# Optimization experiments

Hardware: AMD Instinct MI355X
Metric: run time of the kernel (lower is better)

The kernel has to match this reference:

```python
import jax, jax.numpy as jnp
import numpy as np

B, T, D, H = 8, 4096, 1024, 1024


def setup_inputs() -> dict:
    key = jax.random.key(0)
    ks = jax.random.split(key, 8)
    s = 1.0 / np.sqrt(D)
    x = jax.random.normal(ks[0], (B, T, D), dtype=jnp.float32)
    Wq = jax.random.uniform(ks[1], (H, D), jnp.float32, -s, s)
    bq = jax.random.uniform(ks[2], (H,), jnp.float32, -s, s)
    Wk = jax.random.uniform(ks[3], (H, D), jnp.float32, -s, s)
    bk = jax.random.uniform(ks[4], (H,), jnp.float32, -s, s)
    Wv = jax.random.uniform(ks[5], (H, D), jnp.float32, -s, s)
    bv = jax.random.uniform(ks[6], (H,), jnp.float32, -s, s)
    wbias = jax.random.uniform(ks[7], (H,), jnp.float32, 0.0, 1.0)  # torch.rand
    return {"x": x, "Wq": Wq, "bq": bq, "Wk": Wk, "bk": bk, "Wv": Wv, "bv": bv, "wbias": wbias}


def reference(x, Wq, bq, Wk, bk, Wv, bv, wbias):
    # Q, K, V: [B, T, H]
    Q = jnp.einsum('btd,hd->bth', x, Wq) + bq
    K = jnp.einsum('btd,hd->bth', x, Wk) + bk
    V = jnp.einsum('btd,hd->bth', x, Wv) + bv
    Q_sig = jax.nn.sigmoid(Q)
    numer = jnp.exp(K + wbias)            # [B, T, H]
    denom = numer.sum(axis=0)             # [T, H] (faithful: sum over batch axis)
    weighted = (numer * V).sum(axis=0) / denom  # [T, H]
    Yt = Q_sig * weighted                 # broadcast -> [B, T, H]
    return Yt  # to_out is Identity since dim == hidden_dim
```

## Files before the change

### kernel.cpp

```cpp
#include <hip/hip_runtime.h>
#include <hip/hip_bf16.h>

#define B_ 8
#define T_ 4096
#define D_ 1024
#define H_ 1024

typedef __attribute__((ext_vector_type(8))) short short8;
typedef __attribute__((ext_vector_type(4))) float floatx4;

#define GLOAD16(gptr, lptr) \
  __builtin_amdgcn_global_load_lds((const __attribute__((address_space(1))) void*)(gptr), \
                                   (__attribute__((address_space(3))) void*)(lptr), 16, 0, 0)

__device__ __forceinline__ ushort f2b(float f) {
  unsigned x = __builtin_bit_cast(unsigned, f);
  unsigned r = (x + 0x7fffu + ((x >> 16) & 1u)) >> 16;
  return (ushort)r;
}

__global__ void cvt_kernel(const float* __restrict__ in, ushort* __restrict__ out, int n) {
  int idx = blockIdx.x * blockDim.x + threadIdx.x;
  int stride = gridDim.x * blockDim.x;
  for (long i = (long)idx * 8; i < n; i += (long)stride * 8) {
    const float4 f0 = *(const float4*)(in + i);
    const float4 f1 = *(const float4*)(in + i + 4);
    union { ushort u[8]; uint4 v; } r;
    r.u[0] = f2b(f0.x); r.u[1] = f2b(f0.y); r.u[2] = f2b(f0.z); r.u[3] = f2b(f0.w);
    r.u[4] = f2b(f1.x); r.u[5] = f2b(f1.y); r.u[6] = f2b(f1.z); r.u[7] = f2b(f1.w);
    *(uint4*)(out + i) = r.v;
  }
}

__global__ void cvt3_kernel(const float* __restrict__ w0, const float* __restrict__ w1,
                            const float* __restrict__ w2, ushort* __restrict__ out, int n) {
  const float* in = (blockIdx.y == 0) ? w0 : (blockIdx.y == 1) ? w1 : w2;
  ushort* o = out + (size_t)blockIdx.y * n;
  int idx = blockIdx.x * blockDim.x + threadIdx.x;
  int stride = gridDim.x * blockDim.x;
  for (long i = (long)idx * 8; i < n; i += (long)stride * 8) {
    const float4 f0 = *(const float4*)(in + i);
    const float4 f1 = *(const float4*)(in + i + 4);
    union { ushort u[8]; uint4 v; } r;
    r.u[0] = f2b(f0.x); r.u[1] = f2b(f0.y); r.u[2] = f2b(f0.z); r.u[3] = f2b(f0.w);
    r.u[4] = f2b(f1.x); r.u[5] = f2b(f1.y); r.u[6] = f2b(f1.z); r.u[7] = f2b(f1.w);
    *(uint4*)(o + i) = r.v;
  }
}

__global__ __launch_bounds__(512, 2) void kv_kernel(
    const ushort* __restrict__ xb, const ushort* __restrict__ Wkb,
    const ushort* __restrict__ Wvb, const float* __restrict__ bk,
    const float* __restrict__ bv, const float* __restrict__ wbias,
    float* __restrict__ weighted) {
  extern __shared__ ushort lds[];
  ushort* const AsB = lds;
  ushort* const KsB = lds + 49152;
  ushort* const VsB = lds + 61440;

  const int tid = threadIdx.x;
  const int lane = tid & 63;
  const int w = tid >> 6;
  const int wrow = w >> 1;
  const int wcol = w & 1;

  const int bid = blockIdx.x;
  const int lid = (bid & 7) * 32 + (bid >> 3);
  const int t0 = (lid >> 4) * 256;
  const int h0 = (lid & 15) * 64;

  const int srow = tid >> 3;
  const int swz = (tid & 7) ^ ((tid >> 3) & 7);

  const int arow = wrow * 64 + (lane & 15);
  const int bcol = wcol * 32 + (lane & 15);
  const int cs0 = (lane >> 4) ^ (lane & 7);
  const int cs1 = ((lane >> 4) + 4) ^ (lane & 7);

  float wbc[2], bkc[2], bvc[2];
#pragma unroll
  for (int n = 0; n < 2; ++n) {
    int h = h0 + wcol * 32 + n * 16 + (lane & 15);
    wbc[n] = wbias[h];
    bkc[n] = bk[h];
    bvc[n] = bv[h];
  }

  const ushort* xsb = xb + (size_t)(t0 + srow) * D_ + swz * 8;
  const ushort* ksb = Wkb + (size_t)(h0 + srow) * D_ + swz * 8;
  const ushort* vsb = Wvb + (size_t)(h0 + srow) * D_ + swz * 8;

  auto stage = [&](int p, int nb) {
    const int b = p >> 4;
    const int kt = (p & 15) << 6;
    const ushort* xs = xsb + (size_t)b * (T_ * D_) + kt;
    ushort* Ab = AsB + nb * 16384;
#pragma unroll
    for (int it = 0; it < 4; ++it)
      GLOAD16(xs + (size_t)(it * 64) * D_, Ab + (it * 512 + tid) * 8);
    GLOAD16(ksb + kt, KsB + nb * 4096 + tid * 8);
    GLOAD16(vsb + kt, VsB + nb * 4096 + tid * 8);
  };

  floatx4 accK[4][2] = {};
  floatx4 accV[4][2] = {};
  floatx4 sumN[4][2] = {};
  floatx4 sumWV[4][2] = {};

  stage(0, 0);
  stage(1, 1);
  asm volatile("s_waitcnt vmcnt(6)" ::: "memory");
  __builtin_amdgcn_s_barrier();

  int cur = 0, stg = 2;
  for (int p = 0; p < 128; ++p) {
    if (p < 126) stage(p + 2, stg);

    const ushort* Ac = AsB + cur * 16384;
    const ushort* Kc = KsB + cur * 4096;
    const ushort* Vc = VsB + cur * 4096;
#pragma unroll
    for (int s = 0; s < 2; ++s) {
      const int cs = s ? cs1 : cs0;
      short8 a[4], kb2[2], vb2[2];
#pragma unroll
      for (int m = 0; m < 4; ++m)
        a[m] = *(const short8*)&Ac[(arow + m * 16) * 64 + cs * 8];
#pragma unroll
      for (int n = 0; n < 2; ++n) {
        kb2[n] = *(const short8*)&Kc[(bcol + n * 16) * 64 + cs * 8];
        vb2[n] = *(const short8*)&Vc[(bcol + n * 16) * 64 + cs * 8];
      }
      __builtin_amdgcn_s_setprio(1);
#pragma unroll
      for (int m = 0; m < 4; ++m)
#pragma unroll
        for (int n = 0; n < 2; ++n) {
          accK[m][n] = __builtin_amdgcn_mfma_f32_16x16x32_bf16(a[m], kb2[n], accK[m][n], 0, 0, 0);
          accV[m][n] = __builtin_amdgcn_mfma_f32_16x16x32_bf16(a[m], vb2[n], accV[m][n], 0, 0, 0);
        }
      __builtin_amdgcn_s_setprio(0);
    }

    if ((p & 15) == 15) {
#pragma unroll
      for (int m = 0; m < 4; ++m)
#pragma unroll
        for (int n = 0; n < 2; ++n) {
#pragma unroll
          for (int r = 0; r < 4; ++r) {
            float nmr = __expf(accK[m][n][r] + bkc[n] + wbc[n]);
            sumN[m][n][r] += nmr;
            sumWV[m][n][r] += nmr * (accV[m][n][r] + bvc[n]);
          }
          accK[m][n] = floatx4{0.f, 0.f, 0.f, 0.f};
          accV[m][n] = floatx4{0.f, 0.f, 0.f, 0.f};
        }
    }

    if (p < 126) { asm volatile("s_waitcnt vmcnt(6)" ::: "memory"); }
    else         { asm volatile("s_waitcnt vmcnt(0)" ::: "memory"); }
    __builtin_amdgcn_s_barrier();
    cur = (cur == 2) ? 0 : cur + 1;
    stg = (stg == 2) ? 0 : stg + 1;
  }

#pragma unroll
  for (int m = 0; m < 4; ++m)
#pragma unroll
    for (int n = 0; n < 2; ++n)
#pragma unroll
      for (int r = 0; r < 4; ++r) {
        int t = t0 + wrow * 64 + m * 16 + (lane >> 4) * 4 + r;
        int h = h0 + wcol * 32 + n * 16 + (lane & 15);
        weighted[(size_t)t * H_ + h] = sumWV[m][n][r] / sumN[m][n][r];
      }
}

__global__ __launch_bounds__(512, 2) void q_kernel(
    const ushort* __restrict__ Am, const ushort* __restrict__ Bm,
    const float* __restrict__ bq, const float* __restrict__ weighted,
    float* __restrict__ out) {
  extern __shared__ ushort lds[];

  const int tid = threadIdx.x;
  const int lane = tid & 63;
  const int w = tid >> 6;
  const int wr = w >> 2;
  const int wc = w & 3;

  const int bid = blockIdx.x;
  const int lid = (bid & 7) * 64 + (bid >> 3);
  const int R0 = (lid >> 2) * 256;
  const int C0 = (lid & 3) * 256;

  const int r0 = tid >> 2;
  const int lc = (tid & 3) ^ ((tid >> 3) & 3);
  const ushort* asrc = Am + (size_t)(R0 + r0) * D_ + lc * 8;
  const ushort* bsrc = Bm + (size_t)(C0 + r0) * D_ + lc * 8;

  auto stage = [&](int t) {
    const int nb = t & 3;
    const int kt = t * 32;
    GLOAD16(asrc + kt, lds + nb * 8192 + tid * 8);
    GLOAD16(asrc + kt + (size_t)128 * D_, lds + nb * 8192 + (512 + tid) * 8);
    GLOAD16(bsrc + kt, lds + 32768 + nb * 8192 + tid * 8);
    GLOAD16(bsrc + kt + (size_t)128 * D_, lds + 32768 + nb * 8192 + (512 + tid) * 8);
  };

  const int baseA = wr * 128 + (lane & 15);
  const int baseB = wc * 64 + (lane & 15);
  const int aOff = baseA * 32 + ((lane >> 4) ^ ((baseA >> 1) & 3)) * 8;
  const int bOff = baseB * 32 + ((lane >> 4) ^ ((baseB >> 1) & 3)) * 8;

  floatx4 acc[8][4] = {};

  stage(0); stage(1);
  asm volatile("s_waitcnt vmcnt(4)" ::: "memory");
  __builtin_amdgcn_s_barrier();

  const int NT = D_ / 32;
  for (int t = 0; t < NT; ++t) {
    if (t < NT - 2) stage(t + 2);
    const ushort* Ab = lds + (t & 3) * 8192;
    const ushort* Bb = lds + 32768 + (t & 3) * 8192;

    short8 b[4], a[8];
#pragma unroll
    for (int n = 0; n < 4; ++n) b[n] = *(const short8*)(Bb + bOff + n * 512);
#pragma unroll
    for (int m = 0; m < 8; ++m) a[m] = *(const short8*)(Ab + aOff + m * 512);
#pragma unroll
    for (int m = 0; m < 8; ++m)
#pragma unroll
      for (int n = 0; n < 4; ++n)
        acc[m][n] = __builtin_amdgcn_mfma_f32_16x16x32_bf16(a[m], b[n], acc[m][n], 0, 0, 0);

    if (t < NT - 2) { asm volatile("s_waitcnt vmcnt(4)" ::: "memory"); }
    else            { asm volatile("s_waitcnt vmcnt(0)" ::: "memory"); }
    __builtin_amdgcn_s_barrier();
  }

  const int lrb = wr * 64 + (lane >> 4) * 4;
  const int lcol = wc * 64 + (lane & 15);
#pragma unroll
  for (int mh = 0; mh < 2; ++mh) {
    if (mh) __builtin_amdgcn_s_barrier();
    float* lf = (float*)lds;
#pragma unroll
    for (int mi = 0; mi < 4; ++mi)
#pragma unroll
      for (int n = 0; n < 4; ++n)
#pragma unroll
        for (int r = 0; r < 4; ++r)
          lf[(lrb + mi * 16 + r) * 256 + lcol + n * 16] = acc[mh * 4 + mi][n][r];
    __builtin_amdgcn_s_barrier();
#pragma unroll
    for (int j = 0; j < 16; ++j) {
      int cidx = j * 512 + tid;
      int lr = cidx >> 6;
      int cc = cidx & 63;
      int grow = R0 + (lr >> 6) * 128 + mh * 64 + (lr & 63);
      float4 v = *(float4*)(lf + lr * 256 + cc * 4);
      float4 bq4 = *(const float4*)(bq + C0 + cc * 4);
      float4 wv = *(const float4*)(weighted + (size_t)(grow & (T_ - 1)) * H_ + C0 + cc * 4);
      float4 o;
      o.x = wv.x / (1.f + __expf(-(v.x + bq4.x)));
      o.y = wv.y / (1.f + __expf(-(v.y + bq4.y)));
      o.z = wv.z / (1.f + __expf(-(v.z + bq4.z)));
      o.w = wv.w / (1.f + __expf(-(v.w + bq4.w)));
      *(float4*)(out + (size_t)grow * H_ + C0 + cc * 4) = o;
    }
  }
}

extern "C" void kernel_launch(void* const* d_in, const int* in_sizes, int n_in,
                              void* d_out, int out_size, void* d_ws, size_t ws_size,
                              hipStream_t stream) {
  (void)in_sizes; (void)n_in; (void)out_size; (void)ws_size;
  const float* x = (const float*)d_in[0];
  const float* Wq = (const float*)d_in[1];
  const float* bq = (const float*)d_in[2];
  const float* Wk = (const float*)d_in[3];
  const float* bk = (const float*)d_in[4];
  const float* Wv = (const float*)d_in[5];
  const float* bv = (const float*)d_in[6];
  const float* wbias = (const float*)d_in[7];
  float* out = (float*)d_out;

  char* ws = (char*)d_ws;
  const size_t XN = (size_t)B_ * T_ * D_;
  const size_t WN = (size_t)H_ * D_;
  ushort* xb  = (ushort*)ws;
  ushort* Wqb = (ushort*)(ws + XN * 2);
  ushort* Wkb = Wqb + WN;
  ushort* Wvb = Wkb + WN;
  float* weighted = (float*)(ws + XN * 2 + 3 * WN * 2);

  (void)hipFuncSetAttribute((const void*)kv_kernel,
                            hipFuncAttributeMaxDynamicSharedMemorySize, 147456);
  (void)hipFuncSetAttribute((const void*)q_kernel,
                            hipFuncAttributeMaxDynamicSharedMemorySize, 131072);

  cvt_kernel<<<2048, 256, 0, stream>>>(x, xb, (int)XN);
  cvt3_kernel<<<dim3(512, 3), 256, 0, stream>>>(Wq, Wk, Wv, Wqb, (int)WN);

  kv_kernel<<<256, 512, 147456, stream>>>(xb, Wkb, Wvb, bk, bv, wbias, weighted);
  q_kernel<<<512, 512, 131072, stream>>>(xb, Wqb, bq, weighted, out);
}
```

Baseline: 276.9 us.

## Restage kv_kernel K-tiles to 32 wide covering two batches per stage

```diff
diff --git a/kernel.cpp b/kernel.cpp
--- a/kernel.cpp
+++ b/kernel.cpp
@@ -55,8 +55,7 @@
     float* __restrict__ weighted) {
   extern __shared__ ushort lds[];
   ushort* const AsB = lds;
-  ushort* const KsB = lds + 49152;
-  ushort* const VsB = lds + 61440;
+  ushort* const BsB = lds + 49152;
 
   const int tid = threadIdx.x;
   const int lane = tid & 63;
@@ -69,13 +68,30 @@
   const int t0 = (lid >> 4) * 256;
   const int h0 = (lid & 15) * 64;
 
-  const int srow = tid >> 3;
-  const int swz = (tid & 7) ^ ((tid >> 3) & 7);
-
-  const int arow = wrow * 64 + (lane & 15);
-  const int bcol = wcol * 32 + (lane & 15);
-  const int cs0 = (lane >> 4) ^ (lane & 7);
-  const int cs1 = ((lane >> 4) + 4) ^ (lane & 7);
+  const int rA = tid >> 2;
+  const int lcA = (tid & 3) ^ ((tid >> 3) & 3);
+  const int ci = tid & 255;
+  const int rB = ci >> 2;
+  const int lcB = (ci & 3) ^ ((ci >> 3) & 3);
+
+  const ushort* xsb = xb + (size_t)(t0 + rA) * D_ + lcA * 8;
+  const ushort* wsrc = ((tid < 256) ? Wkb : Wvb) + (size_t)(h0 + rB) * D_ + lcB * 8;
+
+  auto stage = [&](int p, int buf) {
+    const int b0 = (p >> 5) * 2;
+    const int kt = (p & 31) << 5;
+    const ushort* x0 = xsb + (size_t)b0 * (T_ * D_) + kt;
+    ushort* Ab = AsB + buf * 16384;
+    GLOAD16(x0, Ab + tid * 8);
+    GLOAD16(x0 + (size_t)128 * D_, Ab + (512 + tid) * 8);
+    GLOAD16(x0 + (size_t)(T_ * D_), Ab + (1024 + tid) * 8);
+    GLOAD16(x0 + (size_t)(T_ * D_ + 128 * D_), Ab + (1536 + tid) * 8);
+    GLOAD16(wsrc + kt, BsB + buf * 4096 + tid * 8);
+  };
+
+  const int sw = ((lane & 15) >> 1) & 3;
+  const int aBase = (wrow * 64 + (lane & 15)) * 32 + ((lane >> 4) ^ sw) * 8;
+  const int bBase = (wcol * 32 + (lane & 15)) * 32 + ((lane >> 4) ^ sw) * 8;
 
   float wbc[2], bkc[2], bvc[2];
 #pragma unroll
@@ -86,79 +102,62 @@
     bvc[n] = bv[h];
   }
 
-  const ushort* xsb = xb + (size_t)(t0 + srow) * D_ + swz * 8;
-  const ushort* ksb = Wkb + (size_t)(h0 + srow) * D_ + swz * 8;
-  const ushort* vsb = Wvb + (size_t)(h0 + srow) * D_ + swz * 8;
-
-  auto stage = [&](int p, int nb) {
-    const int b = p >> 4;
-    const int kt = (p & 15) << 6;
-    const ushort* xs = xsb + (size_t)b * (T_ * D_) + kt;
-    ushort* Ab = AsB + nb * 16384;
-#pragma unroll
-    for (int it = 0; it < 4; ++it)
-      GLOAD16(xs + (size_t)(it * 64) * D_, Ab + (it * 512 + tid) * 8);
-    GLOAD16(ksb + kt, KsB + nb * 4096 + tid * 8);
-    GLOAD16(vsb + kt, VsB + nb * 4096 + tid * 8);
-  };
-
-  floatx4 accK[4][2] = {};
-  floatx4 accV[4][2] = {};
+  floatx4 accK[2][4][2] = {};
+  floatx4 accV[2][4][2] = {};
   floatx4 sumN[4][2] = {};
   floatx4 sumWV[4][2] = {};
 
   stage(0, 0);
   stage(1, 1);
-  asm volatile("s_waitcnt vmcnt(6)" ::: "memory");
+  asm volatile("s_waitcnt vmcnt(5)" ::: "memory");
   __builtin_amdgcn_s_barrier();
 
   int cur = 0, stg = 2;
   for (int p = 0; p < 128; ++p) {
     if (p < 126) stage(p + 2, stg);
 
-    const ushort* Ac = AsB + cur * 16384;
-    const ushort* Kc = KsB + cur * 4096;
-    const ushort* Vc = VsB + cur * 4096;
-#pragma unroll
-    for (int s = 0; s < 2; ++s) {
-      const int cs = s ? cs1 : cs0;
-      short8 a[4], kb2[2], vb2[2];
+    const ushort* Ab = AsB + cur * 16384;
+    const ushort* Bb = BsB + cur * 4096;
+    short8 kf[2], vf[2], af[4];
+    kf[0] = *(const short8*)(Bb + bBase);
+    kf[1] = *(const short8*)(Bb + bBase + 512);
+    vf[0] = *(const short8*)(Bb + 2048 + bBase);
+    vf[1] = *(const short8*)(Bb + 2048 + bBase + 512);
+#pragma unroll
+    for (int bb = 0; bb < 2; ++bb) {
 #pragma unroll
       for (int m = 0; m < 4; ++m)
-        a[m] = *(const short8*)&Ac[(arow + m * 16) * 64 + cs * 8];
-#pragma unroll
-      for (int n = 0; n < 2; ++n) {
-        kb2[n] = *(const short8*)&Kc[(bcol + n * 16) * 64 + cs * 8];
-        vb2[n] = *(const short8*)&Vc[(bcol + n * 16) * 64 + cs * 8];
-      }
+        af[m] = *(const short8*)(Ab + bb * 8192 + aBase + m * 512);
       __builtin_amdgcn_s_setprio(1);
 #pragma unroll
       for (int m = 0; m < 4; ++m)
 #pragma unroll
         for (int n = 0; n < 2; ++n) {
-          accK[m][n] = __builtin_amdgcn_mfma_f32_16x16x32_bf16(a[m], kb2[n], accK[m][n], 0, 0, 0);
-          accV[m][n] = __builtin_amdgcn_mfma_f32_16x16x32_bf16(a[m], vb2[n], accV[m][n], 0, 0, 0);
+          accK[bb][m][n] = __builtin_amdgcn_mfma_f32_16x16x32_bf16(af[m], kf[n], accK[bb][m][n], 0, 0, 0);
+          accV[bb][m][n] = __builtin_amdgcn_mfma_f32_16x16x32_bf16(af[m], vf[n], accV[bb][m][n], 0, 0, 0);
         }
       __builtin_amdgcn_s_setprio(0);
     }
 
-    if ((p & 15) == 15) {
-#pragma unroll
-      for (int m = 0; m < 4; ++m)
-#pragma unroll
-        for (int n = 0; n < 2; ++n) {
-#pragma unroll
-          for (int r = 0; r < 4; ++r) {
-            float nmr = __expf(accK[m][n][r] + bkc[n] + wbc[n]);
-            sumN[m][n][r] += nmr;
-            sumWV[m][n][r] += nmr * (accV[m][n][r] + bvc[n]);
+    if ((p & 31) == 31) {
+#pragma unroll
+      for (int bb = 0; bb < 2; ++bb)
+#pragma unroll
+        for (int m = 0; m < 4; ++m)
+#pragma unroll
+          for (int n = 0; n < 2; ++n) {
+#pragma unroll
+            for (int r = 0; r < 4; ++r) {
+              float nmr = __expf(accK[bb][m][n][r] + bkc[n] + wbc[n]);
+              sumN[m][n][r] += nmr;
+              sumWV[m][n][r] += nmr * (accV[bb][m][n][r] + bvc[n]);
+            }
+            accK[bb][m][n] = floatx4{0.f, 0.f, 0.f, 0.f};
+            accV[bb][m][n] = floatx4{0.f, 0.f, 0.f, 0.f};
           }
-          accK[m][n] = floatx4{0.f, 0.f, 0.f, 0.f};
-          accV[m][n] = floatx4{0.f, 0.f, 0.f, 0.f};
-        }
     }
 
-    if (p < 126) { asm volatile("s_waitcnt vmcnt(6)" ::: "memory"); }
+    if (p < 126) { asm volatile("s_waitcnt vmcnt(5)" ::: "memory"); }
     else         { asm volatile("s_waitcnt vmcnt(0)" ::: "memory"); }
     __builtin_amdgcn_s_barrier();
     cur = (cur == 2) ? 0 : cur + 1;
@@ -298,13 +297,13 @@
   float* weighted = (float*)(ws + XN * 2 + 3 * WN * 2);
 
   (void)hipFuncSetAttribute((const void*)kv_kernel,
-                            hipFuncAttributeMaxDynamicSharedMemorySize, 147456);
+                            hipFuncAttributeMaxDynamicSharedMemorySize, 122880);
   (void)hipFuncSetAttribute((const void*)q_kernel,
                             hipFuncAttributeMaxDynamicSharedMemorySize, 131072);
 
   cvt_kernel<<<2048, 256, 0, stream>>>(x, xb, (int)XN);
   cvt3_kernel<<<dim3(512, 3), 256, 0, stream>>>(Wq, Wk, Wv, Wqb, (int)WN);
 
-  kv_kernel<<<256, 512, 147456, stream>>>(xb, Wkb, Wvb, bk, bv, wbias, weighted);
+  kv_kernel<<<256, 512, 122880, stream>>>(xb, Wkb, Wvb, bk, bv, wbias, weighted);
   q_kernel<<<512, 512, 131072, stream>>>(xb, Wqb, bq, weighted, out);
 }
```

Result: no change. 275.4 us, median of 2 (-0.5%).

## Shrink KV kernel tiles to 128x64 with 256 threads and static LDS

Applied to the files above, without the earlier changes.

```diff
diff --git a/kernel.cpp b/kernel.cpp
--- a/kernel.cpp
+++ b/kernel.cpp
@@ -48,15 +48,14 @@
   }
 }
 
-__global__ __launch_bounds__(512, 2) void kv_kernel(
+__global__ __launch_bounds__(256, 2) void kv_kernel(
     const ushort* __restrict__ xb, const ushort* __restrict__ Wkb,
     const ushort* __restrict__ Wvb, const float* __restrict__ bk,
     const float* __restrict__ bv, const float* __restrict__ wbias,
     float* __restrict__ weighted) {
-  extern __shared__ ushort lds[];
-  ushort* const AsB = lds;
-  ushort* const KsB = lds + 49152;
-  ushort* const VsB = lds + 61440;
+  __shared__ ushort As[3][128 * 32];
+  __shared__ ushort Ks[3][64 * 32];
+  __shared__ ushort Vs[3][64 * 32];
 
   const int tid = threadIdx.x;
   const int lane = tid & 63;
@@ -65,17 +64,30 @@
   const int wcol = w & 1;
 
   const int bid = blockIdx.x;
-  const int lid = (bid & 7) * 32 + (bid >> 3);
-  const int t0 = (lid >> 4) * 256;
+  const int lid = (bid & 7) * 64 + (bid >> 3);
+  const int t0 = (lid >> 4) * 128;
   const int h0 = (lid & 15) * 64;
 
-  const int srow = tid >> 3;
-  const int swz = (tid & 7) ^ ((tid >> 3) & 7);
-
-  const int arow = wrow * 64 + (lane & 15);
-  const int bcol = wcol * 32 + (lane & 15);
-  const int cs0 = (lane >> 4) ^ (lane & 7);
-  const int cs1 = ((lane >> 4) + 4) ^ (lane & 7);
+  const int rA = tid >> 2;
+  const int lc = (tid & 3) ^ ((tid >> 3) & 3);
+
+  const ushort* xsb = xb + (size_t)(t0 + rA) * D_ + lc * 8;
+  const ushort* ksb = Wkb + (size_t)(h0 + rA) * D_ + lc * 8;
+  const ushort* vsb = Wvb + (size_t)(h0 + rA) * D_ + lc * 8;
+
+  auto stage = [&](int p, int buf) {
+    const int b = p >> 5;
+    const int kt = (p & 31) << 5;
+    const ushort* xs = xsb + (size_t)b * (T_ * D_) + kt;
+    GLOAD16(xs, &As[buf][tid * 8]);
+    GLOAD16(xs + (size_t)64 * D_, &As[buf][(256 + tid) * 8]);
+    GLOAD16(ksb + kt, &Ks[buf][tid * 8]);
+    GLOAD16(vsb + kt, &Vs[buf][tid * 8]);
+  };
+
+  const int sw = ((lane & 15) >> 1) & 3;
+  const int aBase = (wrow * 64 + (lane & 15)) * 32 + ((lane >> 4) ^ sw) * 8;
+  const int bBase = (wcol * 32 + (lane & 15)) * 32 + ((lane >> 4) ^ sw) * 8;
 
   float wbc[2], bkc[2], bvc[2];
 #pragma unroll
@@ -86,22 +98,6 @@
     bvc[n] = bv[h];
   }
 
-  const ushort* xsb = xb + (size_t)(t0 + srow) * D_ + swz * 8;
-  const ushort* ksb = Wkb + (size_t)(h0 + srow) * D_ + swz * 8;
-  const ushort* vsb = Wvb + (size_t)(h0 + srow) * D_ + swz * 8;
-
-  auto stage = [&](int p, int nb) {
-    const int b = p >> 4;
-    const int kt = (p & 15) << 6;
-    const ushort* xs = xsb + (size_t)b * (T_ * D_) + kt;
-    ushort* Ab = AsB + nb * 16384;
-#pragma unroll
-    for (int it = 0; it < 4; ++it)
-      GLOAD16(xs + (size_t)(it * 64) * D_, Ab + (it * 512 + tid) * 8);
-    GLOAD16(ksb + kt, KsB + nb * 4096 + tid * 8);
-    GLOAD16(vsb + kt, VsB + nb * 4096 + tid * 8);
-  };
-
   floatx4 accK[4][2] = {};
   floatx4 accV[4][2] = {};
   floatx4 sumN[4][2] = {};
@@ -109,40 +105,33 @@
 
   stage(0, 0);
   stage(1, 1);
-  asm volatile("s_waitcnt vmcnt(6)" ::: "memory");
+  asm volatile("s_waitcnt vmcnt(4)" ::: "memory");
   __builtin_amdgcn_s_barrier();
 
   int cur = 0, stg = 2;
-  for (int p = 0; p < 128; ++p) {
-    if (p < 126) stage(p + 2, stg);
-
-    const ushort* Ac = AsB + cur * 16384;
-    const ushort* Kc = KsB + cur * 4096;
-    const ushort* Vc = VsB + cur * 4096;
-#pragma unroll
-    for (int s = 0; s < 2; ++s) {
-      const int cs = s ? cs1 : cs0;
-      short8 a[4], kb2[2], vb2[2];
-#pragma unroll
-      for (int m = 0; m < 4; ++m)
-        a[m] = *(const short8*)&Ac[(arow + m * 16) * 64 + cs * 8];
+  for (int p = 0; p < 256; ++p) {
+    if (p < 254) stage(p + 2, stg);
+
+    const ushort* Ac = As[cur];
+    const ushort* Kc = Ks[cur];
+    const ushort* Vc = Vs[cur];
+    short8 a[4], kf[2], vf[2];
+#pragma unroll
+    for (int m = 0; m < 4; ++m) a[m] = *(const short8*)(Ac + aBase + m * 512);
+#pragma unroll
+    for (int n = 0; n < 2; ++n) {
+      kf[n] = *(const short8*)(Kc + bBase + n * 512);
+      vf[n] = *(const short8*)(Vc + bBase + n * 512);
+    }
+#pragma unroll
+    for (int m = 0; m < 4; ++m)
 #pragma unroll
       for (int n = 0; n < 2; ++n) {
-        kb2[n] = *(const short8*)&Kc[(bcol + n * 16) * 64 + cs * 8];
-        vb2[n] = *(const short8*)&Vc[(bcol + n * 16) * 64 + cs * 8];
+        accK[m][n] = __builtin_amdgcn_mfma_f32_16x16x32_bf16(a[m], kf[n], accK[m][n], 0, 0, 0);
+        accV[m][n] = __builtin_amdgcn_mfma_f32_16x16x32_bf16(a[m], vf[n], accV[m][n], 0, 0, 0);
       }
-      __builtin_amdgcn_s_setprio(1);
-#pragma unroll
-      for (int m = 0; m < 4; ++m)
-#pragma unroll
-        for (int n = 0; n < 2; ++n) {
-          accK[m][n] = __builtin_amdgcn_mfma_f32_16x16x32_bf16(a[m], kb2[n], accK[m][n], 0, 0, 0);
-          accV[m][n] = __builtin_amdgcn_mfma_f32_16x16x32_bf16(a[m], vb2[n], accV[m][n], 0, 0, 0);
-        }
-      __builtin_amdgcn_s_setprio(0);
-    }
-
-    if ((p & 15) == 15) {
+
+    if ((p & 31) == 31) {
 #pragma unroll
       for (int m = 0; m < 4; ++m)
 #pragma unroll
@@ -158,7 +147,7 @@
         }
     }
 
-    if (p < 126) { asm volatile("s_waitcnt vmcnt(6)" ::: "memory"); }
+    if (p < 254) { asm volatile("s_waitcnt vmcnt(4)" ::: "memory"); }
     else         { asm volatile("s_waitcnt vmcnt(0)" ::: "memory"); }
     __builtin_amdgcn_s_barrier();
     cur = (cur == 2) ? 0 : cur + 1;
@@ -297,14 +286,12 @@
   ushort* Wvb = Wkb + WN;
   float* weighted = (float*)(ws + XN * 2 + 3 * WN * 2);
 
-  (void)hipFuncSetAttribute((const void*)kv_kernel,
-                            hipFuncAttributeMaxDynamicSharedMemorySize, 147456);
   (void)hipFuncSetAttribute((const void*)q_kernel,
                             hipFuncAttributeMaxDynamicSharedMemorySize, 131072);
 
   cvt_kernel<<<2048, 256, 0, stream>>>(x, xb, (int)XN);
   cvt3_kernel<<<dim3(512, 3), 256, 0, stream>>>(Wq, Wk, Wv, Wqb, (int)WN);
 
-  kv_kernel<<<256, 512, 147456, stream>>>(xb, Wkb, Wvb, bk, bv, wbias, weighted);
+  kv_kernel<<<512, 256, 0, stream>>>(xb, Wkb, Wvb, bk, bv, wbias, weighted);
   q_kernel<<<512, 512, 131072, stream>>>(xb, Wqb, bq, weighted, out);
 }
```

Measured after the change: 321.7 us. 1.16x slower.
